# Kernel optimization log

Hardware: AMD Instinct MI355X
Metric: run time of the kernel (lower is better)

The kernel has to match this reference:

```python
import jax, jax.numpy as jnp
import numpy as np

E = 1024
H = 16
HD = 64
LN_EPS = 1e-5


def _layernorm(x, g, b):
    mu = jnp.mean(x, axis=-1, keepdims=True)
    var = jnp.mean((x - mu) ** 2, axis=-1, keepdims=True)
    return (x - mu) * jax.lax.rsqrt(var + LN_EPS) * g + b


def _positional(L):
    # PositionalEncoding: stepper = 1/10000^(arange(0,E,2)/E); cat(sin, cos) -> [L, E]
    stepper = 1.0 / (10000.0 ** (jnp.arange(0, E, 2, dtype=jnp.float32) / E))
    args = jnp.arange(L, dtype=jnp.float32)[:, None] * stepper[None, :]  # [L, E/2]
    return jnp.concatenate([jnp.sin(args), jnp.cos(args)], axis=1)  # [L, E]


def setup_inputs() -> dict:
    key = jax.random.key(0)
    ks = jax.random.split(key, 8)
    s = 1.0 / np.sqrt(E)
    return {
        "sequences": jax.random.normal(ks[0], (4, 2048, E), dtype=jnp.float32),
        "W_q": jax.random.normal(ks[1], (E, E), dtype=jnp.float32) * s,
        "W_k": jax.random.normal(ks[2], (E, E), dtype=jnp.float32) * s,
        "W_v": jax.random.normal(ks[3], (E, E), dtype=jnp.float32) * s,
        "W_o": jax.random.normal(ks[4], (E, E), dtype=jnp.float32) * s,
        "ln1_g": jnp.ones((E,), jnp.float32),
        "ln1_b": jnp.zeros((E,), jnp.float32),
        "lin_W": jax.random.normal(ks[5], (E, E), dtype=jnp.float32) * s,  # torch Linear weight [out,in]
        "lin_b": jnp.zeros((E,), jnp.float32),
        "ln2_g": jnp.ones((E,), jnp.float32),
        "ln2_b": jnp.zeros((E,), jnp.float32),
    }


def reference(sequences, W_q, W_k, W_v, W_o, ln1_g, ln1_b, lin_W, lin_b, ln2_g, ln2_b):
    B, L, _ = sequences.shape
    x = sequences + _positional(L)[None]  # add positional embeddings
    # projections (no bias)
    q = (x @ W_q).reshape(B, L, H, HD).transpose(0, 2, 1, 3)  # [B,H,L,hd]
    k = (x @ W_k).reshape(B, L, H, HD).transpose(0, 2, 1, 3)
    v = (x @ W_v).reshape(B, L, H, HD).transpose(0, 2, 1, 3)
    # linear (softmax-free) attention: (Q K^T / sqrt(hd)) V
    scores = jnp.einsum("bhqd,bhkd->bhqk", q, k) / jnp.sqrt(jnp.float32(HD))
    ctx = jnp.einsum("bhqk,bhkd->bhqd", scores, v)
    ctx = ctx.transpose(0, 2, 1, 3).reshape(B, L, E)
    attn_out = ctx @ W_o
    h = _layernorm(x + attn_out, ln1_g, ln1_b)
    ff = jax.nn.relu(h @ lin_W.T + lin_b)
    return _layernorm(ff + h, ln2_g, ln2_b)
```

## Files before the change

kernel.cpp:

```cpp
#include <hip/hip_runtime.h>
#include <cstdint>

typedef unsigned short u16;
typedef __bf16 bf16x8 __attribute__((ext_vector_type(8)));
typedef float f32x4 __attribute__((ext_vector_type(4)));

__device__ __forceinline__ u16 f2bf(float f) {
    unsigned u = __float_as_uint(f);
    u += 0x7fffu + ((u >> 16) & 1u);
    return (u16)(u >> 16);
}
__device__ __forceinline__ float bf2f(u16 h) {
    return __uint_as_float(((unsigned)h) << 16);
}

__device__ __forceinline__ void lds16(const void* g, void* l) {
    __builtin_amdgcn_global_load_lds(
        (const __attribute__((address_space(1))) void*)g,
        (__attribute__((address_space(3))) void*)l, 16, 0, 0);
}

__device__ __forceinline__ float pos_term(int l, int e) {
    const float c = -13.287712379549449f / 512.0f;
    int ii = e & 511;
    float st  = exp2f(c * (float)ii);
    float arg = (float)l * st;
    return (e < 512) ? sinf(arg) : cosf(arg);
}

__global__ __launch_bounds__(256) void prep_x(const float* __restrict__ seq,
                                              u16* __restrict__ xb) {
    size_t i = (size_t)blockIdx.x * 256 + threadIdx.x;
    int e4 = (int)(i & 255) * 4;
    int l  = (int)((i >> 8) & 2047);
    float4 s = ((const float4*)seq)[i];
    float v[4] = {s.x, s.y, s.z, s.w};
#pragma unroll
    for (int j = 0; j < 4; j++) v[j] += pos_term(l, e4 + j);
    ushort4 ob; ob.x = f2bf(v[0]); ob.y = f2bf(v[1]); ob.z = f2bf(v[2]); ob.w = f2bf(v[3]);
    ((ushort4*)xb)[i] = ob;
}

__global__ void prep_w(const float* __restrict__ wq, const float* __restrict__ wk,
                       const float* __restrict__ wv, const float* __restrict__ wl,
                       u16* __restrict__ wt) {
    int mat = blockIdx.z;
    const float* src = (mat == 0) ? wq : (mat == 1) ? wk : (mat == 2) ? wv : wl;
    u16* dst = wt + (size_t)mat * 1024 * 1024;
    int tx = threadIdx.x, ty = threadIdx.y;
    if (mat == 0 || mat == 3) {
        int col = blockIdx.x * 32 + tx, row0 = blockIdx.y * 32;
#pragma unroll
        for (int j = 0; j < 32; j += 8)
            dst[(size_t)(row0 + ty + j) * 1024 + col] = f2bf(src[(size_t)(row0 + ty + j) * 1024 + col]);
    } else {
        __shared__ float tile[32][33];
        int col = blockIdx.x * 32 + tx, row0 = blockIdx.y * 32;
#pragma unroll
        for (int j = 0; j < 32; j += 8)
            tile[ty + j][tx] = src[(size_t)(row0 + ty + j) * 1024 + col];
        __syncthreads();
        int col2 = blockIdx.y * 32 + tx, row20 = blockIdx.x * 32;
#pragma unroll
        for (int j = 0; j < 32; j += 8)
            dst[(size_t)(row20 + ty + j) * 1024 + col2] = f2bf(tile[tx][ty + j]);
    }
}

__global__ __launch_bounds__(512) void gemm256(const u16* __restrict__ A,
                                               const u16* __restrict__ Bt,
                                               u16* __restrict__ C,
                                               int N, int K, int lda) {
    __shared__ __align__(16) u16 lds[65536];
    const int t = threadIdx.x;
    const int ntn = N >> 8;
    const int nwg = gridDim.x;
    int bid = (int)blockIdx.x;
    bid = (bid & 7) * (nwg >> 3) + (bid >> 3);
    const int tm = bid / ntn, tn = bid - tm * ntn;
    const size_t m0 = (size_t)tm << 8, n0 = (size_t)tn << 8;
    const int w = t >> 6, lane = t & 63;
    const int wr = w >> 2, wc = w & 3;

    const int r0 = t >> 3;
    const int ksrc = (t & 7) ^ (r0 & 7);
    const u16* sA0 = A + (m0 + r0) * (size_t)lda + ksrc * 8;
    const u16* sA1 = sA0 + (size_t)128 * lda;
    const u16* sB0 = Bt + (n0 + r0) * (size_t)K + ksrc * 8;
    const u16* sB1 = sB0 + (size_t)128 * K;
    const size_t stA = (size_t)64 * lda, stB = (size_t)64 * K;

#define STAGE(bb, hh, src, str, ko)                                           \
    do {                                                                      \
        u16* d_ = lds + (bb) * 32768 + (hh) * 8192 + (w << 9);                \
        lds16((src) + (ko), d_);                                              \
        lds16((src) + (ko) + (str), d_ + 4096);                               \
    } while (0)

    const int kx = lane & 7;
    const int ks0 = (((lane >> 4) ^ kx) << 3);
    const int ks1 = (((4 + (lane >> 4)) ^ kx) << 3);
    const int arow = (wr << 7) + (lane & 15);
    const int brow = (wc << 6) + (lane & 15);

    f32x4 acc[8][4];
#pragma unroll
    for (int i = 0; i < 8; i++)
#pragma unroll
        for (int j = 0; j < 4; j++)
#pragma unroll
            for (int r = 0; r < 4; r++) acc[i][j][r] = 0.0f;

    const int NT = K >> 6;
    STAGE(0, 0, sA0, stA, 0); STAGE(0, 1, sA1, stA, 0);
    STAGE(0, 2, sB0, stB, 0); STAGE(0, 3, sB1, stB, 0);

    for (int kt = 0; kt < NT; kt++) {
        const int b = kt & 1;
        const u16* Lb = lds + b * 32768;
        const size_t ko = (size_t)(kt + 1) << 6;
        const bool pf = (kt + 1 < NT);
        bf16x8 af[4][2], bfr[2][2];
#pragma unroll
        for (int ph = 0; ph < 4; ph++) {
            const int mq = ph >> 1, nq = ph & 1;
            if (ph == 0) {
                if (pf) {
                    STAGE(b ^ 1, 0, sA0, stA, ko);
                    STAGE(b ^ 1, 1, sA1, stA, ko);
                    asm volatile("s_waitcnt vmcnt(4)" ::: "memory");
                } else {
                    asm volatile("s_waitcnt vmcnt(0)" ::: "memory");
                }
                __builtin_amdgcn_s_barrier();
                asm volatile("" ::: "memory");
            }
            if (ph == 0 || ph == 2) {
#pragma unroll
                for (int i = 0; i < 4; i++) {
                    const int ar = (arow + mq * 64 + i * 16) << 6;
                    af[i][0] = *reinterpret_cast<const bf16x8*>(Lb + ar + ks0);
                    af[i][1] = *reinterpret_cast<const bf16x8*>(Lb + ar + ks1);
                }
            }
#pragma unroll
            for (int j = 0; j < 2; j++) {
                const int br = 16384 + ((brow + nq * 32 + j * 16) << 6);
                bfr[j][0] = *reinterpret_cast<const bf16x8*>(Lb + br + ks0);
                bfr[j][1] = *reinterpret_cast<const bf16x8*>(Lb + br + ks1);
            }
            if (ph == 1 && pf) STAGE(b ^ 1, 2, sB0, stB, ko);
            if (ph == 2 && pf) STAGE(b ^ 1, 3, sB1, stB, ko);
            asm volatile("" ::: "memory");
            if (ph != 0) __builtin_amdgcn_s_barrier();
            __builtin_amdgcn_s_setprio(1);
#pragma unroll
            for (int kc = 0; kc < 2; kc++)
#pragma unroll
                for (int i = 0; i < 4; i++)
#pragma unroll
                    for (int j = 0; j < 2; j++)
                        acc[mq * 4 + i][nq * 2 + j] = __builtin_amdgcn_mfma_f32_16x16x32_bf16(
                            af[i][kc], bfr[j][kc], acc[mq * 4 + i][nq * 2 + j], 0, 0, 0);
            __builtin_amdgcn_s_setprio(0);
            asm volatile("" ::: "memory");
            __builtin_amdgcn_s_barrier();
        }
    }
#undef STAGE

    const int crow = (lane >> 4) << 2, ccol = lane & 15;
#pragma unroll
    for (int i = 0; i < 8; i++)
#pragma unroll
        for (int j = 0; j < 4; j++) {
            size_t row = m0 + (wr << 7) + (i << 4) + crow;
            size_t col = n0 + (wc << 6) + (j << 4) + ccol;
#pragma unroll
            for (int r = 0; r < 4; r++)
                C[(row + r) * (size_t)N + col] = f2bf(acc[i][j][r]);
        }
}

template <int EPI>
__global__ __launch_bounds__(512) void gemm8p(const u16* __restrict__ A,
                                              const u16* __restrict__ Bt,
                                              void* __restrict__ Cv,
                                              const float* __restrict__ bias,
                                              int N, int K, int lda, size_t bstride) {
    __shared__ __align__(16) u16 lds[49152];
    const int t = threadIdx.x;
    const int ntn = N >> 8;
    const int nwg = gridDim.x;
    int bid = (int)blockIdx.x;
    bid = (bid & 7) * (nwg >> 3) + (bid >> 3);
    const int tm = bid / ntn, tn = bid - tm * ntn;
    const size_t m0 = (size_t)tm << 7, n0 = (size_t)tn << 8;
    const int w = t >> 6, lane = t & 63;
    const int wr = w >> 2, wc = w & 3;
    const u16* Bt_e = Bt + (bstride ? (m0 >> 11) * bstride : 0);

    const int r0 = t >> 3;
    const int ksrc = (t & 7) ^ (r0 & 7);
    const u16* sA0 = A + (m0 + r0) * (size_t)lda + ksrc * 8;
    const u16* sA1 = sA0 + (size_t)64 * lda;
    const u16* sB0 = Bt_e + (n0 + r0) * (size_t)K + ksrc * 8;
    const u16* sB1 = sB0 + (size_t)64 * K;
    const u16* sB2 = sB0 + (size_t)128 * K;
    const u16* sB3 = sB0 + (size_t)192 * K;
    u16* dstW = lds + (w << 9);

    const int ao = ((wr << 6) | (lane & 15)) << 6;
    const int bo = 8192 + ((((wc << 6) | (lane & 15))) << 6);
    const int kx = lane & 7;
    const int ks0 = (((lane >> 4) ^ kx) << 3);
    const int ks1 = (((4 + (lane >> 4)) ^ kx) << 3);

    f32x4 acc[4][4];
#pragma unroll
    for (int i = 0; i < 4; i++)
#pragma unroll
        for (int j = 0; j < 4; j++)
#pragma unroll
            for (int r = 0; r < 4; r++) acc[i][j][r] = 0.0f;

    const int NT = K >> 6;
    lds16(sA0, dstW);          lds16(sA1, dstW + 4096);
    lds16(sB0, dstW + 8192);   lds16(sB1, dstW + 12288);
    lds16(sB2, dstW + 16384);  lds16(sB3, dstW + 20480);

    for (int kt = 0; kt < NT; kt++) {
        const int b = kt & 1;
        asm volatile("" ::: "memory");
        if (kt + 1 < NT) {
            const size_t ko = (size_t)(kt + 1) << 6;
            u16* d = dstW + (b ^ 1) * 24576;
            lds16(sA0 + ko, d);          lds16(sA1 + ko, d + 4096);
            lds16(sB0 + ko, d + 8192);   lds16(sB1 + ko, d + 12288);
            lds16(sB2 + ko, d + 16384);  lds16(sB3 + ko, d + 20480);
            asm volatile("s_waitcnt vmcnt(6)" ::: "memory");
        } else {
            asm volatile("s_waitcnt vmcnt(0)" ::: "memory");
        }
        __builtin_amdgcn_s_barrier();
        asm volatile("" ::: "memory");
        const u16* Lb = lds + b * 24576;
#pragma unroll
        for (int kc = 0; kc < 2; kc++) {
            const int ksl = kc ? ks1 : ks0;
            bf16x8 af[4], bfr[4];
#pragma unroll
            for (int i = 0; i < 4; i++)
                af[i] = *reinterpret_cast<const bf16x8*>(Lb + ao + i * 1024 + ksl);
#pragma unroll
            for (int j = 0; j < 4; j++)
                bfr[j] = *reinterpret_cast<const bf16x8*>(Lb + bo + j * 1024 + ksl);
            __builtin_amdgcn_s_setprio(1);
#pragma unroll
            for (int i = 0; i < 4; i++)
#pragma unroll
                for (int j = 0; j < 4; j++)
                    acc[i][j] = __builtin_amdgcn_mfma_f32_16x16x32_bf16(af[i], bfr[j], acc[i][j], 0, 0, 0);
            __builtin_amdgcn_s_setprio(0);
        }
        asm volatile("" ::: "memory");
        __builtin_amdgcn_s_barrier();
    }

    const int crow = (lane >> 4) << 2, ccol = lane & 15;
#pragma unroll
    for (int i = 0; i < 4; i++)
#pragma unroll
        for (int j = 0; j < 4; j++) {
            size_t row = m0 + (wr << 6) + (i << 4) + crow;
            size_t col = n0 + (wc << 6) + (j << 4) + ccol;
#pragma unroll
            for (int r = 0; r < 4; r++) {
                float v = acc[i][j][r];
                if (EPI == 3) { v += bias[col]; v = fmaxf(v, 0.0f); }
                ((u16*)Cv)[(row + r) * (size_t)N + col] = f2bf(v);
            }
        }
}

__global__ __launch_bounds__(256) void ktv_kernel(const u16* __restrict__ kv,
                                                  float* __restrict__ part) {
    const int bh = blockIdx.x, split = blockIdx.y;
    const int b = bh >> 4, h = bh & 15;
    const u16* Kp = kv + (size_t)b * 2048 * 2048 + h * 64;
    const u16* Vp = Kp + 1024;
    __shared__ float ks[8][64], vs[8][64];
    float acc[16];
#pragma unroll
    for (int i = 0; i < 16; i++) acc[i] = 0.0f;
    const int t = threadIdx.x, r = t >> 4, c = t & 15;
    const int lr = t >> 5, lc = (t & 31) * 2;
    for (int l0 = split * 128; l0 < split * 128 + 128; l0 += 8) {
        unsigned kk = *(const unsigned*)(Kp + (size_t)(l0 + lr) * 2048 + lc);
        unsigned vv = *(const unsigned*)(Vp + (size_t)(l0 + lr) * 2048 + lc);
        ks[lr][lc] = bf2f((u16)kk); ks[lr][lc + 1] = bf2f((u16)(kk >> 16));
        vs[lr][lc] = bf2f((u16)vv); vs[lr][lc + 1] = bf2f((u16)(vv >> 16));
        __syncthreads();
#pragma unroll
        for (int i = 0; i < 8; i++) {
            float kvr[4], vw[4];
#pragma unroll
            for (int a = 0; a < 4; a++) { kvr[a] = ks[i][r + 16 * a]; vw[a] = vs[i][c + 16 * a]; }
#pragma unroll
            for (int a = 0; a < 4; a++)
#pragma unroll
                for (int q = 0; q < 4; q++) acc[a * 4 + q] += kvr[a] * vw[q];
        }
        __syncthreads();
    }
    float* o = part + ((size_t)split * 64 + bh) * 4096;
#pragma unroll
    for (int a = 0; a < 4; a++)
#pragma unroll
        for (int q = 0; q < 4; q++) o[(r + 16 * a) * 64 + (c + 16 * q)] = acc[a * 4 + q];
}

__global__ __launch_bounds__(256) void ktv_reduce(const float* __restrict__ part,
                                                  float* __restrict__ ktv) {
    int i = blockIdx.x * 256 + threadIdx.x;
    float s = 0.0f;
#pragma unroll
    for (int sp = 0; sp < 16; sp++) s += part[(size_t)sp * 262144 + i];
    ktv[i] = s;
}

__global__ __launch_bounds__(256) void wprime_kernel(const float* __restrict__ ktv,
                                                     const float* __restrict__ Wo,
                                                     u16* __restrict__ wp) {
    const int n = blockIdx.x * 256 + threadIdx.x;
    const int h = blockIdx.y, b = blockIdx.z;
    const float* kt = ktv + ((size_t)(b * 16 + h) << 12);
    float acc[64];
#pragma unroll
    for (int i = 0; i < 64; i++) acc[i] = 0.0f;
    for (int j = 0; j < 64; j++) {
        float w = Wo[(size_t)(h * 64 + j) * 1024 + n];
#pragma unroll
        for (int i = 0; i < 64; i++) acc[i] += kt[i * 64 + j] * w;
    }
    u16* o = wp + ((size_t)b << 20) + (size_t)n * 1024 + h * 64;
    u16 ob[64];
#pragma unroll
    for (int i = 0; i < 64; i++) ob[i] = f2bf(acc[i] * 0.125f);
#pragma unroll
    for (int i = 0; i < 8; i++)
        ((uint4*)o)[i] = ((const uint4*)ob)[i];
}

__global__ __launch_bounds__(256) void ln1_kernel(const u16* __restrict__ xb,
                                                  const u16* __restrict__ attn,
                                                  const float* __restrict__ g,
                                                  const float* __restrict__ be,
                                                  u16* __restrict__ outB) {
    __shared__ float sm[4];
    const int row = blockIdx.x, t = threadIdx.x;
    const ushort4 xv = ((const ushort4*)(xb + (size_t)row * 1024))[t];
    const ushort4 av = ((const ushort4*)(attn + (size_t)row * 1024))[t];
    float x0 = bf2f(xv.x) + bf2f(av.x), x1 = bf2f(xv.y) + bf2f(av.y);
    float x2 = bf2f(xv.z) + bf2f(av.z), x3 = bf2f(xv.w) + bf2f(av.w);
    float s = x0 + x1 + x2 + x3;
#pragma unroll
    for (int off = 32; off > 0; off >>= 1) s += __shfl_down(s, off);
    if ((t & 63) == 0) sm[t >> 6] = s;
    __syncthreads();
    const float mean = (sm[0] + sm[1] + sm[2] + sm[3]) * (1.0f / 1024.0f);
    __syncthreads();
    x0 -= mean; x1 -= mean; x2 -= mean; x3 -= mean;
    float s2 = x0 * x0 + x1 * x1 + x2 * x2 + x3 * x3;
#pragma unroll
    for (int off = 32; off > 0; off >>= 1) s2 += __shfl_down(s2, off);
    if ((t & 63) == 0) sm[t >> 6] = s2;
    __syncthreads();
    const float var = (sm[0] + sm[1] + sm[2] + sm[3]) * (1.0f / 1024.0f);
    const float rs = rsqrtf(var + 1e-5f);
    const float4 gv = ((const float4*)g)[t];
    const float4 bv = ((const float4*)be)[t];
    ushort4 ob;
    ob.x = f2bf(x0 * rs * gv.x + bv.x);
    ob.y = f2bf(x1 * rs * gv.y + bv.y);
    ob.z = f2bf(x2 * rs * gv.z + bv.z);
    ob.w = f2bf(x3 * rs * gv.w + bv.w);
    ((ushort4*)(outB + (size_t)row * 1024))[t] = ob;
}

__global__ __launch_bounds__(256) void ln2_kernel(const u16* __restrict__ ff,
                                                  const u16* __restrict__ h1,
                                                  const float* __restrict__ g,
                                                  const float* __restrict__ be,
                                                  float* __restrict__ outF) {
    __shared__ float sm[4];
    const int row = blockIdx.x, t = threadIdx.x;
    const ushort4 fv = ((const ushort4*)(ff + (size_t)row * 1024))[t];
    const ushort4 hv = ((const ushort4*)(h1 + (size_t)row * 1024))[t];
    float x0 = bf2f(fv.x) + bf2f(hv.x), x1 = bf2f(fv.y) + bf2f(hv.y);
    float x2 = bf2f(fv.z) + bf2f(hv.z), x3 = bf2f(fv.w) + bf2f(hv.w);
    float s = x0 + x1 + x2 + x3;
#pragma unroll
    for (int off = 32; off > 0; off >>= 1) s += __shfl_down(s, off);
    if ((t & 63) == 0) sm[t >> 6] = s;
    __syncthreads();
    const float mean = (sm[0] + sm[1] + sm[2] + sm[3]) * (1.0f / 1024.0f);
    __syncthreads();
    x0 -= mean; x1 -= mean; x2 -= mean; x3 -= mean;
    float s2 = x0 * x0 + x1 * x1 + x2 * x2 + x3 * x3;
#pragma unroll
    for (int off = 32; off > 0; off >>= 1) s2 += __shfl_down(s2, off);
    if ((t & 63) == 0) sm[t >> 6] = s2;
    __syncthreads();
    const float var = (sm[0] + sm[1] + sm[2] + sm[3]) * (1.0f / 1024.0f);
    const float rs = rsqrtf(var + 1e-5f);
    const float4 gv = ((const float4*)g)[t];
    const float4 bv = ((const float4*)be)[t];
    float4 o;
    o.x = x0 * rs * gv.x + bv.x;
    o.y = x1 * rs * gv.y + bv.y;
    o.z = x2 * rs * gv.z + bv.z;
    o.w = x3 * rs * gv.w + bv.w;
    ((float4*)(outF + (size_t)row * 1024))[t] = o;
}

extern "C" void kernel_launch(void* const* d_in, const int* in_sizes, int n_in,
                              void* d_out, int out_size, void* d_ws, size_t ws_size,
                              hipStream_t stream) {
    const float* seq = (const float*)d_in[0];
    const float* Wq  = (const float*)d_in[1];
    const float* Wk  = (const float*)d_in[2];
    const float* Wv  = (const float*)d_in[3];
    const float* Wo  = (const float*)d_in[4];
    const float* g1  = (const float*)d_in[5];
    const float* b1  = (const float*)d_in[6];
    const float* Wl  = (const float*)d_in[7];
    const float* bl  = (const float*)d_in[8];
    const float* g2  = (const float*)d_in[9];
    const float* b2  = (const float*)d_in[10];

    char* ws = (char*)d_ws;
    const size_t MB = 1024 * 1024;
    u16*   x_bf  = (u16*)(ws + 0);
    u16*   wt    = (u16*)(ws + 16 * MB);
    u16*   kv    = (u16*)(ws + 24 * MB);
    float* kpart = (float*)(ws + 56 * MB);
    u16*   attn  = (u16*)(ws + 56 * MB);
    float* ktv   = (float*)(ws + 72 * MB);
    u16*   wpr   = (u16*)(ws + 73 * MB);
    u16*   wcomb = (u16*)(ws + 81 * MB);
    u16*   h1b   = (u16*)(ws + 89 * MB);
    u16*   ffb   = (u16*)(ws + 105 * MB);

    prep_x<<<dim3(8192), dim3(256), 0, stream>>>(seq, x_bf);
    prep_w<<<dim3(32, 32, 4), dim3(32, 8), 0, stream>>>(Wq, Wk, Wv, Wl, wt);
    gemm256<<<dim3(256), dim3(512), 0, stream>>>(x_bf, wt + (size_t)1 * MB, kv,
                                                 2048, 1024, 1024);
    ktv_kernel<<<dim3(64, 16), dim3(256), 0, stream>>>(kv, kpart);
    ktv_reduce<<<dim3(1024), dim3(256), 0, stream>>>(kpart, ktv);
    wprime_kernel<<<dim3(4, 16, 4), dim3(256), 0, stream>>>(ktv, Wo, wpr);
    gemm8p<2><<<dim3(128), dim3(512), 0, stream>>>(wpr, wt, wcomb, nullptr,
                                                   1024, 1024, 1024, 0);
    gemm8p<2><<<dim3(256), dim3(512), 0, stream>>>(x_bf, wcomb, attn, nullptr,
                                                   1024, 1024, 1024, (size_t)1024 * 1024);
    ln1_kernel<<<dim3(8192), dim3(256), 0, stream>>>(x_bf, attn, g1, b1, h1b);
    gemm8p<3><<<dim3(256), dim3(512), 0, stream>>>(h1b, wt + (size_t)3 * MB, ffb,
                                                   bl, 1024, 1024, 1024, 0);
    ln2_kernel<<<dim3(8192), dim3(256), 0, stream>>>(ffb, h1b, g2, b2, (float*)d_out);
}
```

Baseline: 201.8 us.

## Restructure GEMM main loop to prefetch A tiles two steps ahead

```diff
diff --git a/kernel.cpp b/kernel.cpp
--- a/kernel.cpp
+++ b/kernel.cpp
@@ -114,58 +114,118 @@
     const int NT = K >> 6;
     STAGE(0, 0, sA0, stA, 0); STAGE(0, 1, sA1, stA, 0);
     STAGE(0, 2, sB0, stB, 0); STAGE(0, 3, sB1, stB, 0);
+    if (NT > 1) {
+        STAGE(1, 0, sA0, stA, 64); STAGE(1, 1, sA1, stA, 64);
+        asm volatile("s_waitcnt vmcnt(4)" ::: "memory");
+    } else {
+        asm volatile("s_waitcnt vmcnt(0)" ::: "memory");
+    }
+    __builtin_amdgcn_s_barrier();
+    asm volatile("" ::: "memory");
 
     for (int kt = 0; kt < NT; kt++) {
         const int b = kt & 1;
         const u16* Lb = lds + b * 32768;
-        const size_t ko = (size_t)(kt + 1) << 6;
-        const bool pf = (kt + 1 < NT);
-        bf16x8 af[4][2], bfr[2][2];
-#pragma unroll
-        for (int ph = 0; ph < 4; ph++) {
-            const int mq = ph >> 1, nq = ph & 1;
-            if (ph == 0) {
-                if (pf) {
-                    STAGE(b ^ 1, 0, sA0, stA, ko);
-                    STAGE(b ^ 1, 1, sA1, stA, ko);
-                    asm volatile("s_waitcnt vmcnt(4)" ::: "memory");
-                } else {
-                    asm volatile("s_waitcnt vmcnt(0)" ::: "memory");
-                }
-                __builtin_amdgcn_s_barrier();
-                asm volatile("" ::: "memory");
-            }
-            if (ph == 0 || ph == 2) {
-#pragma unroll
-                for (int i = 0; i < 4; i++) {
-                    const int ar = (arow + mq * 64 + i * 16) << 6;
-                    af[i][0] = *reinterpret_cast<const bf16x8*>(Lb + ar + ks0);
-                    af[i][1] = *reinterpret_cast<const bf16x8*>(Lb + ar + ks1);
-                }
-            }
-#pragma unroll
-            for (int j = 0; j < 2; j++) {
-                const int br = 16384 + ((brow + nq * 32 + j * 16) << 6);
-                bfr[j][0] = *reinterpret_cast<const bf16x8*>(Lb + br + ks0);
-                bfr[j][1] = *reinterpret_cast<const bf16x8*>(Lb + br + ks1);
-            }
-            if (ph == 1 && pf) STAGE(b ^ 1, 2, sB0, stB, ko);
-            if (ph == 2 && pf) STAGE(b ^ 1, 3, sB1, stB, ko);
-            asm volatile("" ::: "memory");
-            if (ph != 0) __builtin_amdgcn_s_barrier();
-            __builtin_amdgcn_s_setprio(1);
-#pragma unroll
-            for (int kc = 0; kc < 2; kc++)
-#pragma unroll
-                for (int i = 0; i < 4; i++)
-#pragma unroll
-                    for (int j = 0; j < 2; j++)
-                        acc[mq * 4 + i][nq * 2 + j] = __builtin_amdgcn_mfma_f32_16x16x32_bf16(
-                            af[i][kc], bfr[j][kc], acc[mq * 4 + i][nq * 2 + j], 0, 0, 0);
-            __builtin_amdgcn_s_setprio(0);
-            asm volatile("" ::: "memory");
-            __builtin_amdgcn_s_barrier();
-        }
+        const size_t ko1 = (size_t)(kt + 1) << 6;
+        const size_t ko2 = (size_t)(kt + 2) << 6;
+        const bool p1 = (kt + 1 < NT), p2 = (kt + 2 < NT);
+        bf16x8 af[4][2], b0[2][2], b1[2][2];
+
+#pragma unroll
+        for (int i = 0; i < 4; i++) {
+            const int ar = (arow + i * 16) << 6;
+            af[i][0] = *reinterpret_cast<const bf16x8*>(Lb + ar + ks0);
+            af[i][1] = *reinterpret_cast<const bf16x8*>(Lb + ar + ks1);
+        }
+#pragma unroll
+        for (int j = 0; j < 2; j++) {
+            const int br = 16384 + ((brow + j * 16) << 6);
+            b0[j][0] = *reinterpret_cast<const bf16x8*>(Lb + br + ks0);
+            b0[j][1] = *reinterpret_cast<const bf16x8*>(Lb + br + ks1);
+        }
+        if (p1) STAGE(b ^ 1, 2, sB0, stB, ko1);
+        asm volatile("s_waitcnt lgkmcnt(8)" ::: "memory");
+        __builtin_amdgcn_s_barrier();
+        asm volatile("s_waitcnt lgkmcnt(0)" ::: "memory");
+        __builtin_amdgcn_sched_barrier(0);
+        __builtin_amdgcn_s_setprio(1);
+#pragma unroll
+        for (int kc = 0; kc < 2; kc++)
+#pragma unroll
+            for (int i = 0; i < 4; i++)
+#pragma unroll
+                for (int j = 0; j < 2; j++)
+                    acc[i][j] = __builtin_amdgcn_mfma_f32_16x16x32_bf16(
+                        af[i][kc], b0[j][kc], acc[i][j], 0, 0, 0);
+        __builtin_amdgcn_s_setprio(0);
+        asm volatile("" ::: "memory");
+        __builtin_amdgcn_s_barrier();
+
+#pragma unroll
+        for (int j = 0; j < 2; j++) {
+            const int br = 16384 + ((brow + 32 + j * 16) << 6);
+            b1[j][0] = *reinterpret_cast<const bf16x8*>(Lb + br + ks0);
+            b1[j][1] = *reinterpret_cast<const bf16x8*>(Lb + br + ks1);
+        }
+        if (p1) STAGE(b ^ 1, 3, sB1, stB, ko1);
+        __builtin_amdgcn_s_barrier();
+        asm volatile("s_waitcnt lgkmcnt(0)" ::: "memory");
+        __builtin_amdgcn_sched_barrier(0);
+        __builtin_amdgcn_s_setprio(1);
+#pragma unroll
+        for (int kc = 0; kc < 2; kc++)
+#pragma unroll
+            for (int i = 0; i < 4; i++)
+#pragma unroll
+                for (int j = 0; j < 2; j++)
+                    acc[i][2 + j] = __builtin_amdgcn_mfma_f32_16x16x32_bf16(
+                        af[i][kc], b1[j][kc], acc[i][2 + j], 0, 0, 0);
+        __builtin_amdgcn_s_setprio(0);
+        asm volatile("" ::: "memory");
+        __builtin_amdgcn_s_barrier();
+
+#pragma unroll
+        for (int i = 0; i < 4; i++) {
+            const int ar = (arow + 64 + i * 16) << 6;
+            af[i][0] = *reinterpret_cast<const bf16x8*>(Lb + ar + ks0);
+            af[i][1] = *reinterpret_cast<const bf16x8*>(Lb + ar + ks1);
+        }
+        __builtin_amdgcn_s_barrier();
+        asm volatile("s_waitcnt lgkmcnt(0)" ::: "memory");
+        __builtin_amdgcn_sched_barrier(0);
+        __builtin_amdgcn_s_setprio(1);
+#pragma unroll
+        for (int kc = 0; kc < 2; kc++)
+#pragma unroll
+            for (int i = 0; i < 4; i++)
+#pragma unroll
+                for (int j = 0; j < 2; j++)
+                    acc[4 + i][j] = __builtin_amdgcn_mfma_f32_16x16x32_bf16(
+                        af[i][kc], b0[j][kc], acc[4 + i][j], 0, 0, 0);
+        __builtin_amdgcn_s_setprio(0);
+        asm volatile("" ::: "memory");
+        __builtin_amdgcn_s_barrier();
+
+        if (p2) {
+            STAGE(b, 0, sA0, stA, ko2);
+            STAGE(b, 1, sA1, stA, ko2);
+            asm volatile("s_waitcnt vmcnt(4)" ::: "memory");
+        } else if (p1) {
+            asm volatile("s_waitcnt vmcnt(0)" ::: "memory");
+        }
+        __builtin_amdgcn_s_barrier();
+        __builtin_amdgcn_s_setprio(1);
+#pragma unroll
+        for (int kc = 0; kc < 2; kc++)
+#pragma unroll
+            for (int i = 0; i < 4; i++)
+#pragma unroll
+                for (int j = 0; j < 2; j++)
+                    acc[4 + i][2 + j] = __builtin_amdgcn_mfma_f32_16x16x32_bf16(
+                        af[i][kc], b1[j][kc], acc[4 + i][2 + j], 0, 0, 0);
+        __builtin_amdgcn_s_setprio(0);
+        asm volatile("" ::: "memory");
+        __builtin_amdgcn_s_barrier();
     }
 #undef STAGE
 
```

New measurement: 201.5 us. Within noise of the previous version (-0.2%).
